# Kernel optimization log

Measured on AMD Instinct MI355X. Metric: run time of the kernel, lower is better.

## Reference

```python
import jax, jax.numpy as jnp
import numpy as np

N, E, DIN, H, C = 50000, 800000, 128, 2, 64  # C = hidden_dim*heads (per-head out channels); concat=False -> mean over heads -> layer out dim C
NUM_CLASSES = 4
EPS_GN = 1e-5


def setup_inputs() -> dict:
    key = jax.random.key(0)

    def rn(i, shape, scale):
        return (jax.random.normal(jax.random.fold_in(key, i), shape) * scale).astype(jnp.float32)

    inp = {
        "x": rn(0, (N, DIN), 1.0),
        "edge_index": jax.random.randint(jax.random.fold_in(key, 1), (2, E), 0, N, dtype=jnp.int32),
    }
    layer_in = [DIN, C]
    for li, din in enumerate(layer_in, 1):
        s = 1.0 / np.sqrt(din)
        base = 10 * li
        inp[f"Wl{li}"] = rn(base + 0, (din, H * C), s)
        inp[f"bl{li}"] = jnp.zeros((H * C,), jnp.float32)
        inp[f"Wr{li}"] = rn(base + 1, (din, H * C), s)
        inp[f"br{li}"] = jnp.zeros((H * C,), jnp.float32)
        inp[f"att{li}"] = rn(base + 2, (H, C), 1.0 / np.sqrt(C))
        inp[f"bias{li}"] = jnp.zeros((C,), jnp.float32)
        inp[f"gng{li}"] = jnp.ones((C,), jnp.float32)   # GraphNorm weight
        inp[f"gnb{li}"] = jnp.zeros((C,), jnp.float32)  # GraphNorm bias
        inp[f"gna{li}"] = jnp.ones((C,), jnp.float32)   # GraphNorm mean_scale
    inp["W1"] = rn(100, (C, NUM_CLASSES), 1.0 / np.sqrt(C))
    inp["b1"] = jnp.zeros((NUM_CLASSES,), jnp.float32)
    return inp


def gatv2_layer(x, src, dst, Wl, bl, Wr, br, att, bias):
    # PyG GATv2Conv, concat=False. x: [N, din]
    n = x.shape[0]
    xl = (x @ Wl + bl).reshape(n, H, C)  # source transform
    xr = (x @ Wr + br).reshape(n, H, C)  # target transform
    m = jax.nn.leaky_relu(xl[src] + xr[dst], negative_slope=0.2)  # [E', H, C]
    e = jnp.einsum('ehc,hc->eh', m, att)                           # [E', H]
    emax = jax.lax.stop_gradient(jax.ops.segment_max(e, dst, num_segments=n))
    ee = jnp.exp(e - emax[dst])
    denom = jax.ops.segment_sum(ee, dst, num_segments=n)
    alpha = ee / (denom[dst] + 1e-16)                              # softmax over in-edges of each target
    out = jax.ops.segment_sum(alpha[:, :, None] * xl[src], dst, num_segments=n)  # [N, H, C]
    return out.mean(axis=1) + bias  # concat=False -> mean over heads


def graph_norm(x, gamma, beta, mean_scale):
    # single-graph GraphNorm: stats over all nodes, per feature
    mean = x.mean(axis=0, keepdims=True)
    xc = x - mean_scale * mean
    var = (xc * xc).mean(axis=0, keepdims=True)
    return gamma * xc * jax.lax.rsqrt(var + EPS_GN) + beta


def reference(x, edge_index,
              Wl1, bl1, Wr1, br1, att1, bias1, gng1, gnb1, gna1,
              Wl2, bl2, Wr2, br2, att2, bias2, gng2, gnb2, gna2,
              W1, b1):
    src, dst = edge_index[0], edge_index[1]
    loops = jnp.arange(N, dtype=src.dtype)  # add_self_loops=True
    src = jnp.concatenate([src, loops])
    dst = jnp.concatenate([dst, loops])

    h = gatv2_layer(x, src, dst, Wl1, bl1, Wr1, br1, att1, bias1)
    h = graph_norm(h, gng1, gnb1, gna1)
    h = gatv2_layer(h, src, dst, Wl2, bl2, Wr2, br2, att2, bias2)
    h = graph_norm(h, gng2, gnb2, gna2)

    logits = h @ W1 + b1  # dropout is identity in eval
    return jax.nn.log_softmax(logits, axis=1)
```

## Files before the change

### kernel.cpp

```cpp
#include <hip/hip_runtime.h>
#include <hip/hip_bf16.h>
#include <math.h>

#define HC   128
#define CCH  64
#define NBKE 256

typedef __attribute__((ext_vector_type(8))) short short8;
typedef __attribute__((ext_vector_type(4))) float floatx4;

__device__ __forceinline__ unsigned short f2bf(float f) {
  unsigned u = __float_as_uint(f);
  u += 0x7fffu + ((u >> 16) & 1u);
  return (unsigned short)(u >> 16);
}

__device__ __forceinline__ void unpack8(uint4 u, float* f) {
  f[0] = __uint_as_float(u.x << 16);
  f[1] = __uint_as_float(u.x & 0xffff0000u);
  f[2] = __uint_as_float(u.y << 16);
  f[3] = __uint_as_float(u.y & 0xffff0000u);
  f[4] = __uint_as_float(u.z << 16);
  f[5] = __uint_as_float(u.z & 0xffff0000u);
  f[6] = __uint_as_float(u.w << 16);
  f[7] = __uint_as_float(u.w & 0xffff0000u);
}

template <int CTRL>
__device__ __forceinline__ float dpp_add(float x) {
  int t = __builtin_amdgcn_update_dpp(0, __float_as_int(x), CTRL, 0xf, 0xf, true);
  return x + __int_as_float(t);
}

template <int K>
__device__ __forceinline__ void gemm32rows(
    const unsigned short* __restrict__ A,
    const unsigned short* __restrict__ Wlt, const unsigned short* __restrict__ Wrt,
    const float* __restrict__ bl, const float* __restrict__ br,
    unsigned short* __restrict__ xlb, unsigned short* __restrict__ xrb,
    int M, int row0, int tid) {
  const int w = tid >> 6;
  const int lane = tid & 63;
  const bool isR = w >= 2;
  const unsigned short* Wt = isR ? Wrt : Wlt;
  const float* bias = isR ? br : bl;
  unsigned short* out = isR ? xrb : xlb;
  const int col0 = (w & 1) * 64;
  const int mrow = lane & 15, quad = lane >> 4;
  const unsigned short* pa0 = A + (size_t)(row0 + mrow) * K + quad * 8;
  const unsigned short* pa1 = pa0 + (size_t)16 * K;
  const unsigned short* pb = Wt + (size_t)(col0 + mrow) * K + quad * 8;
  floatx4 acc[2][4];
#pragma unroll
  for (int gp = 0; gp < 2; gp++)
#pragma unroll
    for (int ct = 0; ct < 4; ct++) acc[gp][ct] = (floatx4){0.f, 0.f, 0.f, 0.f};
#pragma unroll
  for (int k0 = 0; k0 < K; k0 += 32) {
    short8 a0 = *(const short8*)(pa0 + k0);
    short8 a1 = *(const short8*)(pa1 + k0);
    short8 b0 = *(const short8*)(pb + k0);
    short8 b1 = *(const short8*)(pb + 16 * K + k0);
    short8 b2 = *(const short8*)(pb + 32 * K + k0);
    short8 b3 = *(const short8*)(pb + 48 * K + k0);
    acc[0][0] = __builtin_amdgcn_mfma_f32_16x16x32_bf16(a0, b0, acc[0][0], 0, 0, 0);
    acc[1][0] = __builtin_amdgcn_mfma_f32_16x16x32_bf16(a1, b0, acc[1][0], 0, 0, 0);
    acc[0][1] = __builtin_amdgcn_mfma_f32_16x16x32_bf16(a0, b1, acc[0][1], 0, 0, 0);
    acc[1][1] = __builtin_amdgcn_mfma_f32_16x16x32_bf16(a1, b1, acc[1][1], 0, 0, 0);
    acc[0][2] = __builtin_amdgcn_mfma_f32_16x16x32_bf16(a0, b2, acc[0][2], 0, 0, 0);
    acc[1][2] = __builtin_amdgcn_mfma_f32_16x16x32_bf16(a1, b2, acc[1][2], 0, 0, 0);
    acc[0][3] = __builtin_amdgcn_mfma_f32_16x16x32_bf16(a0, b3, acc[0][3], 0, 0, 0);
    acc[1][3] = __builtin_amdgcn_mfma_f32_16x16x32_bf16(a1, b3, acc[1][3], 0, 0, 0);
  }
#pragma unroll
  for (int gp = 0; gp < 2; gp++) {
#pragma unroll
    for (int ct = 0; ct < 4; ct++) {
      int col = col0 + ct * 16 + mrow;
      float bv = bias[col];
#pragma unroll
      for (int r = 0; r < 4; r++) {
        int row = row0 + gp * 16 + quad * 4 + r;
        if (row < M) out[(size_t)row * HC + col] = f2bf(acc[gp][ct][r] + bv);
      }
    }
  }
}

__global__ __launch_bounds__(256) void binplace_cast(
    const int* __restrict__ ei, int E, int chunk, int nB, int cap,
    int* __restrict__ gCnt, unsigned* __restrict__ ebuf,
    const float* __restrict__ x, unsigned short* __restrict__ xb, int cnt4,
    const float* __restrict__ Wl, const float* __restrict__ Wr,
    unsigned short* __restrict__ Wlt, unsigned short* __restrict__ Wrt) {
  if ((int)blockIdx.x < NBKE) {
    __shared__ int cnt[512];
    for (int j = threadIdx.x; j < nB; j += 256) cnt[j] = 0;
    __syncthreads();
    int e0 = blockIdx.x * chunk;
    int e1 = e0 + chunk; e1 = e1 < E ? e1 : E;
    int e = e0 + threadIdx.x;
    for (; e + 768 < e1; e += 1024) {
      int d0 = ei[E + e];
      int d1 = ei[E + e + 256];
      int d2 = ei[E + e + 512];
      int d3 = ei[E + e + 768];
      atomicAdd(&cnt[d0 >> 7], 1);
      atomicAdd(&cnt[d1 >> 7], 1);
      atomicAdd(&cnt[d2 >> 7], 1);
      atomicAdd(&cnt[d3 >> 7], 1);
    }
    for (; e < e1; e += 256) atomicAdd(&cnt[ei[E + e] >> 7], 1);
    __syncthreads();
    for (int j = threadIdx.x; j < nB; j += 256) {
      int c = cnt[j];
      int base = c ? atomicAdd(&gCnt[j], c) : 0;
      cnt[j] = j * cap + base;
    }
    __syncthreads();
    e = e0 + threadIdx.x;
    for (; e + 768 < e1; e += 1024) {
      int d0 = ei[E + e];
      int d1 = ei[E + e + 256];
      int d2 = ei[E + e + 512];
      int d3 = ei[E + e + 768];
      int s0 = ei[e];
      int s1 = ei[e + 256];
      int s2 = ei[e + 512];
      int s3 = ei[e + 768];
      int p0 = atomicAdd(&cnt[d0 >> 7], 1);
      int p1 = atomicAdd(&cnt[d1 >> 7], 1);
      int p2 = atomicAdd(&cnt[d2 >> 7], 1);
      int p3 = atomicAdd(&cnt[d3 >> 7], 1);
      ebuf[p0] = (unsigned)s0 | ((unsigned)(d0 & 127) << 16);
      ebuf[p1] = (unsigned)s1 | ((unsigned)(d1 & 127) << 16);
      ebuf[p2] = (unsigned)s2 | ((unsigned)(d2 & 127) << 16);
      ebuf[p3] = (unsigned)s3 | ((unsigned)(d3 & 127) << 16);
    }
    for (; e < e1; e += 256) {
      int dst = ei[E + e];
      int src = ei[e];
      int pos = atomicAdd(&cnt[dst >> 7], 1);
      ebuf[pos] = (unsigned)src | ((unsigned)(dst & 127) << 16);
    }
  } else {
    int gid = (blockIdx.x - NBKE) * 256 + threadIdx.x;
    if (gid < 32768) {
      int sel = gid >> 14;
      int i = gid & 16383;
      int nn = i >> 7, k = i & 127;
      const float* W = sel ? Wr : Wl;
      unsigned short* Wt = sel ? Wrt : Wlt;
      Wt[i] = f2bf(W[k * HC + nn]);
    }
    if (gid >= cnt4) return;
    float4 v = ((const float4*)x)[gid];
    ushort4 o;
    o.x = f2bf(v.x); o.y = f2bf(v.y); o.z = f2bf(v.z); o.w = f2bf(v.w);
    ((ushort4*)xb)[gid] = o;
  }
}

__global__ __launch_bounds__(256) void csr_gemm1(
    const unsigned* __restrict__ ebuf, const int* __restrict__ gCnt, int cap,
    int* __restrict__ row_start, int* __restrict__ deg,
    int* __restrict__ csr_src, int N, int EPtot, int nB,
    const unsigned short* __restrict__ A,
    const unsigned short* __restrict__ Wlt, const unsigned short* __restrict__ Wrt,
    const float* __restrict__ bl, const float* __restrict__ br,
    unsigned short* __restrict__ xlb, unsigned short* __restrict__ xrb, int M) {
  if ((int)blockIdx.x < nB) {
    const int b = blockIdx.x;
    const int tid = threadIdx.x;
    __shared__ int red[256];
    __shared__ int degL[128], scanL[128], curL[128];
    int s = 0;
    for (int k = tid; k < b; k += 256) s += gCnt[k];
    red[tid] = s;
    __syncthreads();
    for (int off = 128; off > 0; off >>= 1) {
      if (tid < off) red[tid] += red[tid + off];
      __syncthreads();
    }
    const int ebase = red[0];
    const int cnt = gCnt[b];
    const int node0 = b * 128;
    const int nb2 = (N - node0) < 128 ? (N - node0) : 128;
    const unsigned* eb = ebuf + (size_t)b * cap;
    if (tid < 128) degL[tid] = 0;
    __syncthreads();
    for (int e = tid; e < cnt; e += 256)
      atomicAdd(&degL[(eb[e] >> 16) & 127], 1);
    __syncthreads();
    if (tid < 128) scanL[tid] = degL[tid];
    __syncthreads();
    for (int off = 1; off < 128; off <<= 1) {
      int t = 0;
      if (tid < 128 && tid >= off) t = scanL[tid - off];
      __syncthreads();
      if (tid < 128) scanL[tid] += t;
      __syncthreads();
    }
    if (tid < 128) {
      int rs = ebase + (scanL[tid] - degL[tid]) + node0 + tid;
      curL[tid] = rs;
      if (tid < nb2) {
        row_start[node0 + tid] = rs;
        deg[node0 + tid] = degL[tid];
      }
    }
    __syncthreads();
    for (int e = tid; e < cnt; e += 256) {
      unsigned p = eb[e];
      int pos = atomicAdd(&curL[(p >> 16) & 127], 1);
      csr_src[pos] = (int)(p & 0xffffu);
    }
    __syncthreads();
    if (tid < nb2) csr_src[curL[tid]] = node0 + tid;
    if (b == 0 && tid < 32) csr_src[EPtot + tid] = 0;
  } else {
    const int row0 = (blockIdx.x - nB) * 32;
    if (row0 >= M) return;
    gemm32rows<128>(A, Wlt, Wrt, bl, br, xlb, xrb, M, row0, threadIdx.x);
  }
}

template <int K>
__global__ __launch_bounds__(256) void gemm_mfma(
    const unsigned short* __restrict__ A,
    const unsigned short* __restrict__ Wlt, const unsigned short* __restrict__ Wrt,
    const float* __restrict__ bl, const float* __restrict__ br,
    unsigned short* __restrict__ xlb, unsigned short* __restrict__ xrb, int M) {
  const int row0 = blockIdx.x * 32;
  if (row0 >= M) return;
  gemm32rows<K>(A, Wlt, Wrt, bl, br, xlb, xrb, M, row0, threadIdx.x);
}

__global__ __launch_bounds__(256) void node_attn(
    const unsigned short* __restrict__ xlb, const unsigned short* __restrict__ xrb,
    const int* __restrict__ csr_src, const int* __restrict__ row_start,
    const int* __restrict__ deg, const float* __restrict__ att,
    const float* __restrict__ bias, unsigned short* __restrict__ outb, int n) {
  int wave = (blockIdx.x * blockDim.x + threadIdx.x) >> 6;
  if (wave >= n) return;
  const int node = wave;
  const int lane = threadIdx.x & 63;
  const int g = lane >> 4;
  const int hl = lane & 15;
  const int c8 = hl << 3;

  float r[8], a[8];
  {
    uint4 u = *(const uint4*)(xrb + (size_t)node * HC + c8);
    unpack8(u, r);
    float4 a0 = *(const float4*)(att + c8);
    float4 a1 = *(const float4*)(att + c8 + 4);
    const float L2E = 1.44269504f;
    a[0] = a0.x * L2E; a[1] = a0.y * L2E; a[2] = a0.z * L2E; a[3] = a0.w * L2E;
    a[4] = a1.x * L2E; a[5] = a1.y * L2E; a[6] = a1.z * L2E; a[7] = a1.w * L2E;
  }

  const int p0 = row_start[node];
  const int pend = p0 + deg[node] + 1;

  float d = 0.f;
  float acc[8] = {0.f, 0.f, 0.f, 0.f, 0.f, 0.f, 0.f, 0.f};

  int s0 = __builtin_nontemporal_load(csr_src + p0 + g);
  uint4 A0 = *(const uint4*)(xlb + (size_t)s0 * HC + c8);
  int s1 = __builtin_nontemporal_load(csr_src + p0 + 4 + g);
  uint4 A1 = *(const uint4*)(xlb + (size_t)s1 * HC + c8);
  int s2 = __builtin_nontemporal_load(csr_src + p0 + 8 + g);
  uint4 A2 = *(const uint4*)(xlb + (size_t)s2 * HC + c8);

  for (int p = p0; p < pend; p += 4) {
    int s3 = __builtin_nontemporal_load(csr_src + p + 12 + g);
    uint4 A3 = *(const uint4*)(xlb + (size_t)s3 * HC + c8);

    float v[8];
    unpack8(A0, v);
    float e1 = 0.f, e2 = 0.f;
#pragma unroll
    for (int i = 0; i < 8; i++) {
      float s = v[i] + r[i];
      e1 = fmaf(a[i], s, e1);
      e2 = fmaf(a[i], fabsf(s), e2);
    }
    float e = fmaf(0.4f, e2, 0.6f * e1);
    e = dpp_add<0xB1>(e);
    e = dpp_add<0x4E>(e);
    e = dpp_add<0x141>(e);

    bool valid = (p + g) < pend;
    float w = valid ? exp2f(e) : 0.f;
    d += w;
#pragma unroll
    for (int i = 0; i < 8; i++) acc[i] = fmaf(w, v[i], acc[i]);
    A0 = A1; A1 = A2; A2 = A3;
  }

#pragma unroll
  for (int ofs = 16; ofs <= 32; ofs <<= 1) {
    d += __shfl_xor(d, ofs);
#pragma unroll
    for (int i = 0; i < 8; i++) acc[i] += __shfl_xor(acc[i], ofs);
  }
  float inv = 1.f / (d + 1e-16f);
  const float* bb = bias + (c8 & 63);
  float o[8];
#pragma unroll
  for (int i = 0; i < 8; i++) {
    float t = acc[i] * inv;
    float t2 = __shfl_xor(t, 8);
    o[i] = 0.5f * (t + t2) + bb[i];
  }
  if (lane < 8) {
    uint4 ou;
    ou.x = (unsigned)f2bf(o[0]) | ((unsigned)f2bf(o[1]) << 16);
    ou.y = (unsigned)f2bf(o[2]) | ((unsigned)f2bf(o[3]) << 16);
    ou.z = (unsigned)f2bf(o[4]) | ((unsigned)f2bf(o[5]) << 16);
    ou.w = (unsigned)f2bf(o[6]) | ((unsigned)f2bf(o[7]) << 16);
    *(uint4*)(outb + (size_t)node * CCH + c8) = ou;
  }
}

__global__ __launch_bounds__(256) void gn_stats(
    const unsigned short* __restrict__ y, float* __restrict__ S, int n) {
  __shared__ float l1a[256], l1b[256], l2a[256], l2b[256];
  int half = threadIdx.x & 31;
  int sub = threadIdx.x >> 5;
  float s1a = 0.f, s1b = 0.f, s2a = 0.f, s2b = 0.f;
  int stride = gridDim.x * 8;
  for (int r = blockIdx.x * 8 + sub; r < n; r += stride) {
    unsigned u = ((const unsigned*)(y + (size_t)r * CCH))[half];
    float va = __uint_as_float(u << 16);
    float vb = __uint_as_float(u & 0xffff0000u);
    s1a += va; s2a = fmaf(va, va, s2a);
    s1b += vb; s2b = fmaf(vb, vb, s2b);
  }
  l1a[threadIdx.x] = s1a; l1b[threadIdx.x] = s1b;
  l2a[threadIdx.x] = s2a; l2b[threadIdx.x] = s2b;
  __syncthreads();
  if (threadIdx.x < 32) {
#pragma unroll
    for (int k = 1; k < 8; k++) {
      s1a += l1a[threadIdx.x + 32 * k];
      s1b += l1b[threadIdx.x + 32 * k];
      s2a += l2a[threadIdx.x + 32 * k];
      s2b += l2b[threadIdx.x + 32 * k];
    }
    atomicAdd(&S[2 * half], s1a);
    atomicAdd(&S[2 * half + 1], s1b);
    atomicAdd(&S[64 + 2 * half], s2a);
    atomicAdd(&S[64 + 2 * half + 1], s2b);
  }
}

__global__ __launch_bounds__(256) void gn_stats_prep(
    const unsigned short* __restrict__ y, float* __restrict__ S,
    int* __restrict__ done, const float* __restrict__ gamma,
    const float* __restrict__ beta, const float* __restrict__ mscale,
    const float* __restrict__ Wl2, const float* __restrict__ bl2,
    const float* __restrict__ Wr2, const float* __restrict__ br2,
    unsigned short* __restrict__ Wl2tb, float* __restrict__ bl2p,
    unsigned short* __restrict__ Wr2tb, float* __restrict__ br2p, int n) {
  __shared__ float l1a[256], l1b[256], l2a[256], l2b[256];
  int half = threadIdx.x & 31;
  int sub = threadIdx.x >> 5;
  float s1a = 0.f, s1b = 0.f, s2a = 0.f, s2b = 0.f;
  int stride = gridDim.x * 8;
  for (int r = blockIdx.x * 8 + sub; r < n; r += stride) {
    unsigned u = ((const unsigned*)(y + (size_t)r * CCH))[half];
    float va = __uint_as_float(u << 16);
    float vb = __uint_as_float(u & 0xffff0000u);
    s1a += va; s2a = fmaf(va, va, s2a);
    s1b += vb; s2b = fmaf(vb, vb, s2b);
  }
  l1a[threadIdx.x] = s1a; l1b[threadIdx.x] = s1b;
  l2a[threadIdx.x] = s2a; l2b[threadIdx.x] = s2b;
  __syncthreads();
  if (threadIdx.x < 32) {
#pragma unroll
    for (int k = 1; k < 8; k++) {
      s1a += l1a[threadIdx.x + 32 * k];
      s1b += l1b[threadIdx.x + 32 * k];
      s2a += l2a[threadIdx.x + 32 * k];
      s2b += l2b[threadIdx.x + 32 * k];
    }
    atomicAdd(&S[2 * half], s1a);
    atomicAdd(&S[2 * half + 1], s1b);
    atomicAdd(&S[64 + 2 * half], s2a);
    atomicAdd(&S[64 + 2 * half + 1], s2b);
  }
  __threadfence();
  __shared__ int isLast;
  if (threadIdx.x == 0) {
    int old = atomicAdd(done, 1);
    isLast = (old == (int)gridDim.x - 1) ? 1 : 0;
  }
  __syncthreads();
  if (!isLast) return;
  __threadfence();
  __shared__ float As[64], Bs[64];
  int t = threadIdx.x;
  if (t < 64) {
    float invn = 1.f / (float)n;
    float mu = S[t] * invn;
    float ms = mscale[t];
    float var = S[64 + t] * invn - 2.f * ms * mu * mu + ms * ms * mu * mu;
    float A = gamma[t] * rsqrtf(var + 1e-5f);
    As[t] = A;
    Bs[t] = beta[t] - A * ms * mu;
  }
  __syncthreads();
  const int side = t >> 7, col = t & 127;
  const float* W = side ? Wr2 : Wl2;
  unsigned short* Wt = side ? Wr2tb : Wl2tb;
  const float* bin = side ? br2 : bl2;
  float* bout = side ? br2p : bl2p;
  float s = 0.f;
  for (int c = 0; c < 64; c++) {
    float w = W[c * HC + col];
    Wt[col * 64 + c] = f2bf(As[c] * w);
    s = fmaf(Bs[c], w, s);
  }
  bout[col] = bin[col] + s;
}

__global__ __launch_bounds__(256) void classify(
    const unsigned short* __restrict__ h,
    const float* __restrict__ S, const float* __restrict__ gamma,
    const float* __restrict__ beta, const float* __restrict__ mscale,
    const float* __restrict__ W, const float* __restrict__ b,
    float* __restrict__ out, int n) {
  __shared__ float4 sW[64];
  __shared__ float sBt[256];
  __shared__ float sb[4];
  int tid = threadIdx.x;
  if (tid < 64) {
    float invn = 1.f / (float)n;
    float mu = S[tid] * invn;
    float ms = mscale[tid];
    float var = S[64 + tid] * invn - 2.f * ms * mu * mu + ms * ms * mu * mu;
    float A = gamma[tid] * rsqrtf(var + 1e-5f);
    float B = beta[tid] - A * ms * mu;
    float4 w = ((const float4*)W)[tid];
    sW[tid] = make_float4(A * w.x, A * w.y, A * w.z, A * w.w);
    sBt[tid * 4 + 0] = B * w.x; sBt[tid * 4 + 1] = B * w.y;
    sBt[tid * 4 + 2] = B * w.z; sBt[tid * 4 + 3] = B * w.w;
  }
  __syncthreads();
  if (tid < 4) {
    float s = b[tid];
    for (int c = 0; c < 64; c++) s += sBt[c * 4 + tid];
    sb[tid] = s;
  }
  __syncthreads();
  int node = blockIdx.x * 256 + tid;
  if (node >= n) return;
  float acc0 = sb[0], acc1 = sb[1], acc2 = sb[2], acc3 = sb[3];
  const uint4* row = (const uint4*)(h + (size_t)node * CCH);
#pragma unroll
  for (int k4 = 0; k4 < 8; k4++) {
    uint4 u = row[k4];
    float v[8];
    unpack8(u, v);
#pragma unroll
    for (int j = 0; j < 8; j++) {
      float4 w = sW[k4 * 8 + j];
      acc0 = fmaf(v[j], w.x, acc0);
      acc1 = fmaf(v[j], w.y, acc1);
      acc2 = fmaf(v[j], w.z, acc2);
      acc3 = fmaf(v[j], w.w, acc3);
    }
  }
  float mx = fmaxf(fmaxf(acc0, acc1), fmaxf(acc2, acc3));
  float s = __expf(acc0 - mx) + __expf(acc1 - mx) + __expf(acc2 - mx) + __expf(acc3 - mx);
  float lse = mx + logf(s);
  float4 o = make_float4(acc0 - lse, acc1 - lse, acc2 - lse, acc3 - lse);
  *((float4*)(out + (size_t)node * 4)) = o;
}

extern "C" void kernel_launch(void* const* d_in, const int* in_sizes, int n_in,
                              void* d_out, int out_size, void* d_ws, size_t ws_size,
                              hipStream_t stream) {
  const float* x     = (const float*)d_in[0];
  const int*   ei    = (const int*)d_in[1];
  const float* Wl1   = (const float*)d_in[2];
  const float* bl1   = (const float*)d_in[3];
  const float* Wr1   = (const float*)d_in[4];
  const float* br1   = (const float*)d_in[5];
  const float* att1  = (const float*)d_in[6];
  const float* bias1 = (const float*)d_in[7];
  const float* gng1  = (const float*)d_in[8];
  const float* gnb1  = (const float*)d_in[9];
  const float* gna1  = (const float*)d_in[10];
  const float* Wl2   = (const float*)d_in[11];
  const float* bl2   = (const float*)d_in[12];
  const float* Wr2   = (const float*)d_in[13];
  const float* br2   = (const float*)d_in[14];
  const float* att2  = (const float*)d_in[15];
  const float* bias2 = (const float*)d_in[16];
  const float* gng2  = (const float*)d_in[17];
  const float* gnb2  = (const float*)d_in[18];
  const float* gna2  = (const float*)d_in[19];
  const float* W1    = (const float*)d_in[20];
  const float* b1    = (const float*)d_in[21];

  const int N = in_sizes[0] / 128;
  const int E = in_sizes[1] / 2;
  const int EP = E + N;
  const int nB = (N + 127) >> 7;
  const int chunk = (E + NBKE - 1) / NBKE;
  const int cap = ((E / nB) * 2 + 255) & ~255;

  int* gCnt = (int*)d_ws;
  float* S1  = (float*)(gCnt + 512);
  float* S2  = S1 + 128;
  int* done  = (int*)(S2 + 128);
  float* bl2p = (float*)(done + 64);
  float* br2p = bl2p + 128;
  unsigned short* xb    = (unsigned short*)(br2p + 128);
  unsigned short* xlb   = xb + (size_t)N * HC;
  unsigned short* xrb   = xlb + (size_t)N * HC;
  unsigned short* aggb  = xrb + (size_t)N * HC;
  unsigned short* Wl1tb = aggb + (size_t)N * CCH;
  unsigned short* Wr1tb = Wl1tb + HC * HC;
  unsigned short* Wl2tb = Wr1tb + HC * HC;
  unsigned short* Wr2tb = Wl2tb + HC * CCH;
  int* row_st  = (int*)(Wr2tb + HC * CCH);
  int* deg     = row_st + N;
  unsigned* ebuf = (unsigned*)(deg + N);
  int* csr_src = (int*)(ebuf + (size_t)nB * cap);

  dim3 b256(256);
  const int gNode = (N * 64 + 255) / 256;
  const int gCls  = (N + 255) / 256;
  const int gCast = (N * 32 + 255) / 256;
  const int gGemm = (N + 31) / 32;

  hipMemsetAsync(d_ws, 0, 4096, stream);

  binplace_cast<<<NBKE + gCast, b256, 0, stream>>>(
      ei, E, chunk, nB, cap, gCnt, ebuf,
      x, xb, N * 32, Wl1, Wr1, Wl1tb, Wr1tb);

  csr_gemm1<<<nB + gGemm, b256, 0, stream>>>(
      ebuf, gCnt, cap, row_st, deg, csr_src, N, EP, nB,
      xb, Wl1tb, Wr1tb, bl1, br1, xlb, xrb, N);

  node_attn<<<gNode, b256, 0, stream>>>(xlb, xrb, csr_src, row_st, deg, att1, bias1, aggb, N);
  gn_stats_prep<<<256, b256, 0, stream>>>(aggb, S1, done, gng1, gnb1, gna1,
                                          Wl2, bl2, Wr2, br2,
                                          Wl2tb, bl2p, Wr2tb, br2p, N);

  gemm_mfma<64><<<gGemm, b256, 0, stream>>>(aggb, Wl2tb, Wr2tb, bl2p, br2p, xlb, xrb, N);
  node_attn<<<gNode, b256, 0, stream>>>(xlb, xrb, csr_src, row_st, deg, att2, bias2, aggb, N);
  gn_stats<<<256, b256, 0, stream>>>(aggb, S2, N);

  classify<<<gCls, b256, 0, stream>>>(aggb, S2, gng2, gnb2, gna2, W1, b1,
                                      (float*)d_out, N);
}
```

Measured before the change: 316.5 us.

## Build CSR with per-node global atomics instead of two-pass bucket sort

Replaces the bucket-then-local-sort CSR construction with a per-node degree count using global atomics, a block-sum plus scan kernel pair, and a direct scatter of source ids into the CSR via per-node cursor atomics. This removes the intermediate edge bucket buffer and its second read pass, but adds two small kernel launches and heavy global atomic contention on 50k counters. Self-loop placement moves to the scan kernel, and the placement still overlaps with the first GEMM in a shared launch.

```diff
diff --git a/kernel.cpp b/kernel.cpp
--- a/kernel.cpp
+++ b/kernel.cpp
@@ -87,16 +87,13 @@
   }
 }
 
-__global__ __launch_bounds__(256) void binplace_cast(
-    const int* __restrict__ ei, int E, int chunk, int nB, int cap,
-    int* __restrict__ gCnt, unsigned* __restrict__ ebuf,
+__global__ __launch_bounds__(256) void deg_cast(
+    const int* __restrict__ ei, int E, int chunk,
+    int* __restrict__ deg,
     const float* __restrict__ x, unsigned short* __restrict__ xb, int cnt4,
     const float* __restrict__ Wl, const float* __restrict__ Wr,
     unsigned short* __restrict__ Wlt, unsigned short* __restrict__ Wrt) {
   if ((int)blockIdx.x < NBKE) {
-    __shared__ int cnt[512];
-    for (int j = threadIdx.x; j < nB; j += 256) cnt[j] = 0;
-    __syncthreads();
     int e0 = blockIdx.x * chunk;
     int e1 = e0 + chunk; e1 = e1 < E ? e1 : E;
     int e = e0 + threadIdx.x;
@@ -105,20 +102,92 @@
       int d1 = ei[E + e + 256];
       int d2 = ei[E + e + 512];
       int d3 = ei[E + e + 768];
-      atomicAdd(&cnt[d0 >> 7], 1);
-      atomicAdd(&cnt[d1 >> 7], 1);
-      atomicAdd(&cnt[d2 >> 7], 1);
-      atomicAdd(&cnt[d3 >> 7], 1);
-    }
-    for (; e < e1; e += 256) atomicAdd(&cnt[ei[E + e] >> 7], 1);
+      atomicAdd(&deg[d0], 1);
+      atomicAdd(&deg[d1], 1);
+      atomicAdd(&deg[d2], 1);
+      atomicAdd(&deg[d3], 1);
+    }
+    for (; e < e1; e += 256) atomicAdd(&deg[ei[E + e]], 1);
+  } else {
+    int gid = (blockIdx.x - NBKE) * 256 + threadIdx.x;
+    if (gid < 32768) {
+      int sel = gid >> 14;
+      int i = gid & 16383;
+      int nn = i >> 7, k = i & 127;
+      const float* W = sel ? Wr : Wl;
+      unsigned short* Wt = sel ? Wrt : Wlt;
+      Wt[i] = f2bf(W[k * HC + nn]);
+    }
+    if (gid >= cnt4) return;
+    float4 v = ((const float4*)x)[gid];
+    ushort4 o;
+    o.x = f2bf(v.x); o.y = f2bf(v.y); o.z = f2bf(v.z); o.w = f2bf(v.w);
+    ((ushort4*)xb)[gid] = o;
+  }
+}
+
+__global__ __launch_bounds__(128) void bucket_sum(
+    const int* __restrict__ deg, int* __restrict__ blkSum, int N) {
+  int i = blockIdx.x * 128 + threadIdx.x;
+  int v = (i < N) ? deg[i] : 0;
+#pragma unroll
+  for (int o = 32; o >= 1; o >>= 1) v += __shfl_xor(v, o);
+  __shared__ int ws[2];
+  if ((threadIdx.x & 63) == 0) ws[threadIdx.x >> 6] = v;
+  __syncthreads();
+  if (threadIdx.x == 0) blkSum[blockIdx.x] = ws[0] + ws[1];
+}
+
+__global__ __launch_bounds__(128) void row_scan(
+    const int* __restrict__ deg, const int* __restrict__ blkSum,
+    int* __restrict__ row_start, int* __restrict__ cur,
+    int* __restrict__ csr_src, int N, int EPtot) {
+  const int b = blockIdx.x;
+  const int tid = threadIdx.x;
+  const int node0 = b * 128;
+  __shared__ int red[128];
+  int s = 0;
+  for (int k = tid; k < b; k += 128) s += blkSum[k];
+  red[tid] = s;
+  __syncthreads();
+  for (int off = 64; off > 0; off >>= 1) {
+    if (tid < off) red[tid] += red[tid + off];
     __syncthreads();
-    for (int j = threadIdx.x; j < nB; j += 256) {
-      int c = cnt[j];
-      int base = c ? atomicAdd(&gCnt[j], c) : 0;
-      cnt[j] = j * cap + base;
-    }
+  }
+  const int ebase = red[0];
+  __syncthreads();
+  const int node = node0 + tid;
+  const int dv = (node < N) ? deg[node] : 0;
+  red[tid] = dv;
+  __syncthreads();
+  for (int off = 1; off < 128; off <<= 1) {
+    int t = 0;
+    if (tid >= off) t = red[tid - off];
     __syncthreads();
-    e = e0 + threadIdx.x;
+    red[tid] += t;
+    __syncthreads();
+  }
+  const int excl = red[tid] - dv;
+  if (node < N) {
+    int rs = ebase + excl + node;
+    row_start[node] = rs;
+    cur[node] = rs;
+    csr_src[rs + dv] = node;
+  }
+  if (b == 0 && tid < 32) csr_src[EPtot + tid] = 0;
+}
+
+__global__ __launch_bounds__(256) void place_gemm1(
+    const int* __restrict__ ei, int E, int chunk,
+    int* __restrict__ cur, int* __restrict__ csr_src,
+    const unsigned short* __restrict__ A,
+    const unsigned short* __restrict__ Wlt, const unsigned short* __restrict__ Wrt,
+    const float* __restrict__ bl, const float* __restrict__ br,
+    unsigned short* __restrict__ xlb, unsigned short* __restrict__ xrb, int M) {
+  if ((int)blockIdx.x < NBKE) {
+    int e0 = blockIdx.x * chunk;
+    int e1 = e0 + chunk; e1 = e1 < E ? e1 : E;
+    int e = e0 + threadIdx.x;
     for (; e + 768 < e1; e += 1024) {
       int d0 = ei[E + e];
       int d1 = ei[E + e + 256];
@@ -128,98 +197,22 @@
       int s1 = ei[e + 256];
       int s2 = ei[e + 512];
       int s3 = ei[e + 768];
-      int p0 = atomicAdd(&cnt[d0 >> 7], 1);
-      int p1 = atomicAdd(&cnt[d1 >> 7], 1);
-      int p2 = atomicAdd(&cnt[d2 >> 7], 1);
-      int p3 = atomicAdd(&cnt[d3 >> 7], 1);
-      ebuf[p0] = (unsigned)s0 | ((unsigned)(d0 & 127) << 16);
-      ebuf[p1] = (unsigned)s1 | ((unsigned)(d1 & 127) << 16);
-      ebuf[p2] = (unsigned)s2 | ((unsigned)(d2 & 127) << 16);
-      ebuf[p3] = (unsigned)s3 | ((unsigned)(d3 & 127) << 16);
+      int p0 = atomicAdd(&cur[d0], 1);
+      int p1 = atomicAdd(&cur[d1], 1);
+      int p2 = atomicAdd(&cur[d2], 1);
+      int p3 = atomicAdd(&cur[d3], 1);
+      csr_src[p0] = s0;
+      csr_src[p1] = s1;
+      csr_src[p2] = s2;
+      csr_src[p3] = s3;
     }
     for (; e < e1; e += 256) {
       int dst = ei[E + e];
       int src = ei[e];
-      int pos = atomicAdd(&cnt[dst >> 7], 1);
-      ebuf[pos] = (unsigned)src | ((unsigned)(dst & 127) << 16);
+      csr_src[atomicAdd(&cur[dst], 1)] = src;
     }
   } else {
-    int gid = (blockIdx.x - NBKE) * 256 + threadIdx.x;
-    if (gid < 32768) {
-      int sel = gid >> 14;
-      int i = gid & 16383;
-      int nn = i >> 7, k = i & 127;
-      const float* W = sel ? Wr : Wl;
-      unsigned short* Wt = sel ? Wrt : Wlt;
-      Wt[i] = f2bf(W[k * HC + nn]);
-    }
-    if (gid >= cnt4) return;
-    float4 v = ((const float4*)x)[gid];
-    ushort4 o;
-    o.x = f2bf(v.x); o.y = f2bf(v.y); o.z = f2bf(v.z); o.w = f2bf(v.w);
-    ((ushort4*)xb)[gid] = o;
-  }
-}
-
-__global__ __launch_bounds__(256) void csr_gemm1(
-    const unsigned* __restrict__ ebuf, const int* __restrict__ gCnt, int cap,
-    int* __restrict__ row_start, int* __restrict__ deg,
-    int* __restrict__ csr_src, int N, int EPtot, int nB,
-    const unsigned short* __restrict__ A,
-    const unsigned short* __restrict__ Wlt, const unsigned short* __restrict__ Wrt,
-    const float* __restrict__ bl, const float* __restrict__ br,
-    unsigned short* __restrict__ xlb, unsigned short* __restrict__ xrb, int M) {
-  if ((int)blockIdx.x < nB) {
-    const int b = blockIdx.x;
-    const int tid = threadIdx.x;
-    __shared__ int red[256];
-    __shared__ int degL[128], scanL[128], curL[128];
-    int s = 0;
-    for (int k = tid; k < b; k += 256) s += gCnt[k];
-    red[tid] = s;
-    __syncthreads();
-    for (int off = 128; off > 0; off >>= 1) {
-      if (tid < off) red[tid] += red[tid + off];
-      __syncthreads();
-    }
-    const int ebase = red[0];
-    const int cnt = gCnt[b];
-    const int node0 = b * 128;
-    const int nb2 = (N - node0) < 128 ? (N - node0) : 128;
-    const unsigned* eb = ebuf + (size_t)b * cap;
-    if (tid < 128) degL[tid] = 0;
-    __syncthreads();
-    for (int e = tid; e < cnt; e += 256)
-      atomicAdd(&degL[(eb[e] >> 16) & 127], 1);
-    __syncthreads();
-    if (tid < 128) scanL[tid] = degL[tid];
-    __syncthreads();
-    for (int off = 1; off < 128; off <<= 1) {
-      int t = 0;
-      if (tid < 128 && tid >= off) t = scanL[tid - off];
-      __syncthreads();
-      if (tid < 128) scanL[tid] += t;
-      __syncthreads();
-    }
-    if (tid < 128) {
-      int rs = ebase + (scanL[tid] - degL[tid]) + node0 + tid;
-      curL[tid] = rs;
-      if (tid < nb2) {
-        row_start[node0 + tid] = rs;
-        deg[node0 + tid] = degL[tid];
-      }
-    }
-    __syncthreads();
-    for (int e = tid; e < cnt; e += 256) {
-      unsigned p = eb[e];
-      int pos = atomicAdd(&curL[(p >> 16) & 127], 1);
-      csr_src[pos] = (int)(p & 0xffffu);
-    }
-    __syncthreads();
-    if (tid < nb2) csr_src[curL[tid]] = node0 + tid;
-    if (b == 0 && tid < 32) csr_src[EPtot + tid] = 0;
-  } else {
-    const int row0 = (blockIdx.x - nB) * 32;
+    const int row0 = (blockIdx.x - NBKE) * 32;
     if (row0 >= M) return;
     gemm32rows<128>(A, Wlt, Wrt, bl, br, xlb, xrb, M, row0, threadIdx.x);
   }
@@ -512,14 +505,16 @@
   const int EP = E + N;
   const int nB = (N + 127) >> 7;
   const int chunk = (E + NBKE - 1) / NBKE;
-  const int cap = ((E / nB) * 2 + 255) & ~255;
-
-  int* gCnt = (int*)d_ws;
-  float* S1  = (float*)(gCnt + 512);
+
+  float* S1  = (float*)d_ws;
   float* S2  = S1 + 128;
   int* done  = (int*)(S2 + 128);
-  float* bl2p = (float*)(done + 64);
-  float* br2p = bl2p + 128;
+  int* deg   = (int*)d_ws + 512;
+  int* cur     = deg + N;
+  int* row_st  = cur + N;
+  int* blkSum  = row_st + N;
+  float* bl2p  = (float*)(blkSum + 512);
+  float* br2p  = bl2p + 128;
   unsigned short* xb    = (unsigned short*)(br2p + 128);
   unsigned short* xlb   = xb + (size_t)N * HC;
   unsigned short* xrb   = xlb + (size_t)N * HC;
@@ -528,10 +523,7 @@
   unsigned short* Wr1tb = Wl1tb + HC * HC;
   unsigned short* Wl2tb = Wr1tb + HC * HC;
   unsigned short* Wr2tb = Wl2tb + HC * CCH;
-  int* row_st  = (int*)(Wr2tb + HC * CCH);
-  int* deg     = row_st + N;
-  unsigned* ebuf = (unsigned*)(deg + N);
-  int* csr_src = (int*)(ebuf + (size_t)nB * cap);
+  int* csr_src = (int*)(Wr2tb + HC * CCH);
 
   dim3 b256(256);
   const int gNode = (N * 64 + 255) / 256;
@@ -539,14 +531,16 @@
   const int gCast = (N * 32 + 255) / 256;
   const int gGemm = (N + 31) / 32;
 
-  hipMemsetAsync(d_ws, 0, 4096, stream);
-
-  binplace_cast<<<NBKE + gCast, b256, 0, stream>>>(
-      ei, E, chunk, nB, cap, gCnt, ebuf,
-      x, xb, N * 32, Wl1, Wr1, Wl1tb, Wr1tb);
-
-  csr_gemm1<<<nB + gGemm, b256, 0, stream>>>(
-      ebuf, gCnt, cap, row_st, deg, csr_src, N, EP, nB,
+  hipMemsetAsync(d_ws, 0, 2048 + (size_t)N * 4, stream);
+
+  deg_cast<<<NBKE + gCast, b256, 0, stream>>>(
+      ei, E, chunk, deg, x, xb, N * 32, Wl1, Wr1, Wl1tb, Wr1tb);
+
+  bucket_sum<<<nB, dim3(128), 0, stream>>>(deg, blkSum, N);
+  row_scan<<<nB, dim3(128), 0, stream>>>(deg, blkSum, row_st, cur, csr_src, N, EP);
+
+  place_gemm1<<<NBKE + gGemm, b256, 0, stream>>>(
+      ei, E, chunk, cur, csr_src,
       xb, Wl1tb, Wr1tb, bl1, br1, xlb, xrb, N);
 
   node_attn<<<gNode, b256, 0, stream>>>(xlb, xrb, csr_src, row_st, deg, att1, bias1, aggb, N);
```

Result: slower. 382.8 us (+20.9%).
